# Kernel tuning notes

Measured on AMD Instinct MI355X. Metric: run time of the kernel, lower is better.

The kernel has to match this reference:

```python
import jax, jax.numpy as jnp
import numpy as np

H = 64       # hidden_size
V = 200000   # vocab_size
B = 1024     # batch (sessions)
N = 50       # unique nodes per session graph
S = 50       # session sequence length


def setup_inputs() -> dict:
    key = jax.random.key(0)
    ks = jax.random.split(key, 24)
    s = 0.05
    lin = lambda k, i, o: jax.random.normal(k, (i, o), jnp.float32) * s  # stored [in,out]
    return {
        "alias_inputs": jax.random.randint(ks[0], (B, S), 0, N),
        "ain": jax.random.uniform(ks[1], (B, N, N), jnp.float32) * 0.1,
        "aou": jax.random.uniform(ks[2], (B, N, N), jnp.float32) * 0.1,
        "items": jax.random.randint(ks[3], (B, N), 0, V),
        "mask": jnp.ones((B, S), jnp.int32),
        "edge_index": jnp.zeros((2, 1), jnp.int32),
        "emb": jax.random.normal(ks[4], (V, H), jnp.float32) * s,
        "ein_w": lin(ks[5], H, H), "ein_b": jnp.zeros((H,), jnp.float32),
        "eou_w": lin(ks[6], H, H), "eou_b": jnp.zeros((H,), jnp.float32),
        "b_iah": jax.random.normal(ks[7], (H,), jnp.float32) * s,
        "b_oah": jax.random.normal(ks[8], (H,), jnp.float32) * s,
        "igate_w": lin(ks[9], 2 * H, 3 * H), "igate_b": jnp.zeros((3 * H,), jnp.float32),
        "hgate_w": lin(ks[10], H, 3 * H), "hgate_b": jnp.zeros((3 * H,), jnp.float32),
        "fc1_w": lin(ks[11], H, H), "fc1_b": jnp.zeros((H,), jnp.float32),
        "fc2_w": lin(ks[12], H, H), "fc2_b": jnp.zeros((H,), jnp.float32),
        "fc3_w": lin(ks[13], H, 1),
    }


def _forward(alias_inputs, ain, aou, items, mask, emb,
             ein_w, ein_b, eou_w, eou_b, b_iah, b_oah,
             igate_w, igate_b, hgate_w, hgate_b,
             fc1_w, fc1_b, fc2_w, fc2_b, fc3_w):
    STEP = 1
    h = emb[items]  # [B,N,H]
    for _ in range(STEP):
        # GRU-style gated graph conv cell
        input_in = jnp.matmul(ain, h @ ein_w + ein_b) + b_iah    # [B,N,H]
        input_out = jnp.matmul(aou, h @ eou_w + eou_b) + b_oah   # [B,N,H]
        inputs = jnp.concatenate([input_in, input_out], axis=-1)  # [B,N,2H]
        gi = inputs @ igate_w + igate_b                          # [B,N,3H]
        gh = h @ hgate_w + hgate_b                               # [B,N,3H]
        i_r, i_i, i_n = jnp.split(gi, 3, axis=-1)
        h_r, h_i, h_n = jnp.split(gh, 3, axis=-1)
        resetgate = jax.nn.sigmoid(i_r + h_r)
        inputgate = jax.nn.sigmoid(i_i + h_i)
        newgate = jnp.tanh(i_n + resetgate * h_n)
        h = newgate + inputgate * (h - newgate)
    # batch_emb: gather node states back to sequence order
    seq = jnp.take_along_axis(h, alias_inputs[..., None], axis=1)  # [B,S,H]
    # attention readout
    last = jnp.sum(mask, axis=1) - 1                               # [B]
    ht = seq[jnp.arange(seq.shape[0]), last]                       # [B,H]
    q1 = (ht @ fc1_w + fc1_b)[:, None, :]                          # [B,1,H]
    q2 = seq @ fc2_w + fc2_b                                       # [B,S,H]
    alpha = jax.nn.sigmoid(q1 + q2) @ fc3_w                        # [B,S,1]
    a = jnp.sum(alpha * seq * mask[..., None].astype(seq.dtype), axis=1)  # [B,H]
    return a @ emb[1:].T                                           # [B,V-1]


def reference(alias_inputs, ain, aou, items, mask, edge_index, emb,
              ein_w, ein_b, eou_w, eou_b, b_iah, b_oah,
              igate_w, igate_b, hgate_w, hgate_b,
              fc1_w, fc1_b, fc2_w, fc2_b, fc3_w):
    del edge_index  # unused in the original forward
    return _forward(alias_inputs, ain, aou, items, mask, emb,
                    ein_w, ein_b, eou_w, eou_b, b_iah, b_oah,
                    igate_w, igate_b, hgate_w, hgate_b,
                    fc1_w, fc1_b, fc2_w, fc2_b, fc3_w)
```

## Files before the change

kernel.cpp:

```cpp
#include <hip/hip_runtime.h>
#include <math.h>

#define H 64
#define N 50
#define S 50
#define B 1024
#define V 200000
#define VO (V - 1)

__global__ __launch_bounds__(256) void k1_embed_lin(
    const int* __restrict__ items, const float* __restrict__ emb,
    const float* __restrict__ ein_w, const float* __restrict__ ein_b,
    const float* __restrict__ eou_w, const float* __restrict__ eou_b,
    float* __restrict__ h0, float* __restrict__ hv_in, float* __restrict__ hv_out)
{
    int tid = threadIdx.x;
    int j = tid & 63, w = tid >> 6;
    int bn0 = blockIdx.x * 32;
    __shared__ __align__(16) float hs[32][H];

    for (int idx = tid; idx < 32 * H; idx += 256) {
        int row = idx >> 6, col = idx & 63;
        int item = items[bn0 + row];
        float hv = emb[(size_t)item * H + col];
        hs[row][col] = hv;
        h0[(size_t)(bn0 + row) * H + col] = hv;
    }
    __syncthreads();

    float accI[8], accO[8];
    {
        float bi = ein_b[j], bo = eou_b[j];
        #pragma unroll
        for (int r = 0; r < 8; r++) { accI[r] = bi; accO[r] = bo; }
    }
    int base = w * 8;
    #pragma unroll 4
    for (int k4 = 0; k4 < 16; k4++) {
        float4 xv[8];
        #pragma unroll
        for (int r = 0; r < 8; r++)
            xv[r] = *(const float4*)&hs[base + r][k4 * 4];
        #pragma unroll
        for (int kk = 0; kk < 4; kk++) {
            int k = k4 * 4 + kk;
            float wi = ein_w[k * H + j];
            float wo = eou_w[k * H + j];
            #pragma unroll
            for (int r = 0; r < 8; r++) {
                float x = ((const float*)&xv[r])[kk];
                accI[r] += x * wi;
                accO[r] += x * wo;
            }
        }
    }
    #pragma unroll
    for (int r = 0; r < 8; r++) {
        hv_in [(size_t)(bn0 + base + r) * H + j] = accI[r];
        hv_out[(size_t)(bn0 + base + r) * H + j] = accO[r];
    }
}

__global__ __launch_bounds__(256) void k2_adj(
    const float* __restrict__ ain, const float* __restrict__ aou,
    const float* __restrict__ hv_in, const float* __restrict__ hv_out,
    const float* __restrict__ b_iah, const float* __restrict__ b_oah,
    float* __restrict__ in_in, float* __restrict__ in_out)
{
    int tid = threadIdx.x;
    int j = tid & 63, w = tid >> 6;
    int b = blockIdx.x;
    __shared__ float hin_s[N][H];
    __shared__ float hou_s[N][H];

    for (int idx = tid; idx < N * H; idx += 256) {
        int row = idx >> 6, col = idx & 63;
        hin_s[row][col] = hv_in [((size_t)b * N + row) * H + col];
        hou_s[row][col] = hv_out[((size_t)b * N + row) * H + col];
    }
    __syncthreads();

    float bi = b_iah[j], bo = b_oah[j];
    for (int n = w; n < N; n += 4) {
        const float* ar = ain + ((size_t)b * N + n) * N;
        const float* br = aou + ((size_t)b * N + n) * N;
        float si = bi, so = bo;
        for (int m = 0; m < N; m++) {
            si += ar[m] * hin_s[m][j];
            so += br[m] * hou_s[m][j];
        }
        in_in [((size_t)b * N + n) * H + j] = si;
        in_out[((size_t)b * N + n) * H + j] = so;
    }
}

__global__ __launch_bounds__(256) void k3_gru(
    const float* __restrict__ in_in, const float* __restrict__ in_out,
    const float* __restrict__ igate_w, const float* __restrict__ igate_b,
    const float* __restrict__ hgate_w, const float* __restrict__ hgate_b,
    float* __restrict__ h0)
{
    int tid = threadIdx.x;
    int j = tid & 63, w = tid >> 6;
    int bn0 = blockIdx.x * 32;
    __shared__ __align__(16) float inp_s[32][2 * H];
    __shared__ __align__(16) float h_s[32][H];

    for (int idx = tid; idx < 32 * H; idx += 256) {
        int row = idx >> 6, col = idx & 63;
        size_t g = (size_t)(bn0 + row) * H + col;
        inp_s[row][col]     = in_in[g];
        inp_s[row][H + col] = in_out[g];
        h_s[row][col]       = h0[g];
    }
    __syncthreads();

    int base = w * 8;
    float gr[8], gi[8], gn[8];
    {
        float b0v = igate_b[j], b1v = igate_b[H + j], b2v = igate_b[2 * H + j];
        #pragma unroll
        for (int r = 0; r < 8; r++) { gr[r] = b0v; gi[r] = b1v; gn[r] = b2v; }
    }
    #pragma unroll 2
    for (int k4 = 0; k4 < 32; k4++) {
        float4 xv[8];
        #pragma unroll
        for (int r = 0; r < 8; r++)
            xv[r] = *(const float4*)&inp_s[base + r][k4 * 4];
        #pragma unroll
        for (int kk = 0; kk < 4; kk++) {
            int k = k4 * 4 + kk;
            const float* wrow = igate_w + (size_t)k * 3 * H;
            float w0 = wrow[j], w1 = wrow[H + j], w2 = wrow[2 * H + j];
            #pragma unroll
            for (int r = 0; r < 8; r++) {
                float x = ((const float*)&xv[r])[kk];
                gr[r] += x * w0; gi[r] += x * w1; gn[r] += x * w2;
            }
        }
    }
    float hr[8], hi[8], hn[8];
    {
        float b0v = hgate_b[j], b1v = hgate_b[H + j], b2v = hgate_b[2 * H + j];
        #pragma unroll
        for (int r = 0; r < 8; r++) { hr[r] = b0v; hi[r] = b1v; hn[r] = b2v; }
    }
    #pragma unroll 2
    for (int k4 = 0; k4 < 16; k4++) {
        float4 xv[8];
        #pragma unroll
        for (int r = 0; r < 8; r++)
            xv[r] = *(const float4*)&h_s[base + r][k4 * 4];
        #pragma unroll
        for (int kk = 0; kk < 4; kk++) {
            int k = k4 * 4 + kk;
            const float* wrow = hgate_w + (size_t)k * 3 * H;
            float w0 = wrow[j], w1 = wrow[H + j], w2 = wrow[2 * H + j];
            #pragma unroll
            for (int r = 0; r < 8; r++) {
                float x = ((const float*)&xv[r])[kk];
                hr[r] += x * w0; hi[r] += x * w1; hn[r] += x * w2;
            }
        }
    }
    #pragma unroll
    for (int r = 0; r < 8; r++) {
        float resetg = 1.f / (1.f + expf(-(gr[r] + hr[r])));
        float inputg = 1.f / (1.f + expf(-(gi[r] + hi[r])));
        float newg = tanhf(gn[r] + resetg * hn[r]);
        float h = h_s[base + r][j];
        h0[(size_t)(bn0 + base + r) * H + j] = newg + inputg * (h - newg);
    }
}

__global__ __launch_bounds__(256) void k4_attn(
    const int* __restrict__ alias_in, const int* __restrict__ mask,
    const float* __restrict__ h,
    const float* __restrict__ fc1_w, const float* __restrict__ fc1_b,
    const float* __restrict__ fc2_w, const float* __restrict__ fc2_b,
    const float* __restrict__ fc3_w, float* __restrict__ a)
{
    int tid = threadIdx.x;
    int j = tid & 63, w = tid >> 6;
    int b = blockIdx.x;
    __shared__ __align__(16) float seq_s[S][H];
    __shared__ float f2s[H][H];
    __shared__ float q1s[H];
    __shared__ float apart[4][H];
    __shared__ int msum_s;

    for (int idx = tid; idx < S * H; idx += 256) {
        int s = idx >> 6, c = idx & 63;
        int node = alias_in[b * S + s];
        seq_s[s][c] = h[((size_t)b * N + node) * H + c];
    }
    for (int idx = tid; idx < H * H; idx += 256)
        f2s[idx >> 6][idx & 63] = fc2_w[idx];
    if (tid == 0) {
        int m = 0;
        for (int s = 0; s < S; s++) m += mask[b * S + s];
        msum_s = m;
    }
    __syncthreads();

    int last = msum_s - 1;
    if (w == 0) {
        float q1 = fc1_b[j];
        for (int k = 0; k < H; k++) q1 += seq_s[last][k] * fc1_w[k * H + j];
        q1s[j] = q1;
    }
    __syncthreads();

    float f3 = fc3_w[j];
    float q1v = q1s[j];
    float aj = 0.f;
    for (int s = w; s < S; s += 4) {
        float q2 = fc2_b[j];
        #pragma unroll 4
        for (int k4 = 0; k4 < 16; k4++) {
            float4 sv = *(const float4*)&seq_s[s][k4 * 4];
            q2 += sv.x * f2s[k4 * 4 + 0][j] + sv.y * f2s[k4 * 4 + 1][j]
                + sv.z * f2s[k4 * 4 + 2][j] + sv.w * f2s[k4 * 4 + 3][j];
        }
        float v = (1.f / (1.f + expf(-(q1v + q2)))) * f3;
        #pragma unroll
        for (int off = 1; off < 64; off <<= 1) v += __shfl_xor(v, off, 64);
        aj += v * seq_s[s][j] * (float)mask[b * S + s];
    }
    apart[w][j] = aj;
    __syncthreads();
    if (w == 0)
        a[b * H + j] = apart[0][j] + apart[1][j] + apart[2][j] + apart[3][j];
}

__global__ __launch_bounds__(256) void k5_out(
    const float* __restrict__ a, const float* __restrict__ emb,
    float* __restrict__ out)
{
    __shared__ __align__(16) float As[128][68];
    __shared__ __align__(16) float Es[128][68];
    int tid = threadIdx.x;
    int tx = tid & 15, ty = tid >> 4;
    int v0 = blockIdx.x * 128;
    int b0 = blockIdx.y * 128;

    for (int idx = tid; idx < 128 * 16; idx += 256) {
        int row = idx >> 4, k4 = idx & 15;
        *(float4*)&As[row][k4 * 4] =
            *(const float4*)(a + (size_t)(b0 + row) * H + k4 * 4);
        int v = v0 + row;
        float4 ev = make_float4(0.f, 0.f, 0.f, 0.f);
        if (v < VO) ev = *(const float4*)(emb + (size_t)(v + 1) * H + k4 * 4);
        *(float4*)&Es[row][k4 * 4] = ev;
    }
    __syncthreads();

    float acc[8][8] = {};
    #pragma unroll 2
    for (int k4 = 0; k4 < 16; k4++) {
        float4 af[8], ef[8];
        #pragma unroll
        for (int i = 0; i < 8; i++)
            af[i] = *(const float4*)&As[ty + 16 * i][k4 * 4];
        #pragma unroll
        for (int jj = 0; jj < 8; jj++)
            ef[jj] = *(const float4*)&Es[tx + 16 * jj][k4 * 4];
        #pragma unroll
        for (int i = 0; i < 8; i++)
            #pragma unroll
            for (int jj = 0; jj < 8; jj++)
                acc[i][jj] += af[i].x * ef[jj].x + af[i].y * ef[jj].y +
                              af[i].z * ef[jj].z + af[i].w * ef[jj].w;
    }

    if (v0 + 128 <= VO) {
        #pragma unroll
        for (int i = 0; i < 8; i++) {
            size_t bofs = (size_t)(b0 + ty + 16 * i) * VO;
            #pragma unroll
            for (int jj = 0; jj < 8; jj++)
                out[bofs + v0 + tx + 16 * jj] = acc[i][jj];
        }
    } else {
        #pragma unroll
        for (int i = 0; i < 8; i++) {
            size_t bofs = (size_t)(b0 + ty + 16 * i) * VO;
            #pragma unroll
            for (int jj = 0; jj < 8; jj++) {
                int v = v0 + tx + 16 * jj;
                if (v < VO) out[bofs + v] = acc[i][jj];
            }
        }
    }
}

extern "C" void kernel_launch(void* const* d_in, const int* in_sizes, int n_in,
                              void* d_out, int out_size, void* d_ws, size_t ws_size,
                              hipStream_t stream)
{
    const int*   alias_in = (const int*)d_in[0];
    const float* ain      = (const float*)d_in[1];
    const float* aou      = (const float*)d_in[2];
    const int*   items    = (const int*)d_in[3];
    const int*   mask     = (const int*)d_in[4];
    const float* emb      = (const float*)d_in[6];
    const float* ein_w    = (const float*)d_in[7];
    const float* ein_b    = (const float*)d_in[8];
    const float* eou_w    = (const float*)d_in[9];
    const float* eou_b    = (const float*)d_in[10];
    const float* b_iah    = (const float*)d_in[11];
    const float* b_oah    = (const float*)d_in[12];
    const float* igate_w  = (const float*)d_in[13];
    const float* igate_b  = (const float*)d_in[14];
    const float* hgate_w  = (const float*)d_in[15];
    const float* hgate_b  = (const float*)d_in[16];
    const float* fc1_w    = (const float*)d_in[17];
    const float* fc1_b    = (const float*)d_in[18];
    const float* fc2_w    = (const float*)d_in[19];
    const float* fc2_b    = (const float*)d_in[20];
    const float* fc3_w    = (const float*)d_in[21];

    float* out = (float*)d_out;

    const size_t NH = (size_t)B * N * H;
    float* h0     = out;
    float* hv_in  = h0 + NH;
    float* hv_out = hv_in + NH;
    float* in_in  = hv_out + NH;
    float* in_out = in_in + NH;
    float* a      = (float*)d_ws;

    k1_embed_lin<<<(B * N) / 32, 256, 0, stream>>>(items, emb, ein_w, ein_b,
                                                   eou_w, eou_b, h0, hv_in, hv_out);
    k2_adj<<<B, 256, 0, stream>>>(ain, aou, hv_in, hv_out, b_iah, b_oah,
                                  in_in, in_out);
    k3_gru<<<(B * N) / 32, 256, 0, stream>>>(in_in, in_out, igate_w, igate_b,
                                             hgate_w, hgate_b, h0);
    k4_attn<<<B, 256, 0, stream>>>(alias_in, mask, h0, fc1_w, fc1_b,
                                   fc2_w, fc2_b, fc3_w, a);
    dim3 g5((VO + 127) / 128, B / 128);
    k5_out<<<g5, 256, 0, stream>>>(a, emb, out);
}
```

Measured before the change: 1.413 ms.

## Use split-bf16 MFMA for the final vocab projection GEMM

The output projection a @ emb[1:].T now runs on MFMA matrix cores instead of FP32 FMAs. Each fp32 operand is split into a bf16 high part and a bf16 low residual, and three cross products (hi*hi, lo*hi, hi*lo) are accumulated with the 16x16x32 bf16 MFMA to approximate fp32 accuracy. The goal is to cut the compute cost of the large B x V GEMM. In exchange the staging loop does extra conversion work, and the result is slightly less accurate than a full fp32 product. The output is about 800 MB of fp32 writes, so store bandwidth may still set the runtime.

Measured after the change: 1.314 ms. 1.08x faster.

```diff
diff --git a/kernel.cpp b/kernel.cpp
--- a/kernel.cpp
+++ b/kernel.cpp
@@ -7,6 +7,20 @@
 #define B 1024
 #define V 200000
 #define VO (V - 1)
+
+typedef __attribute__((ext_vector_type(8))) short short8v;
+typedef __attribute__((ext_vector_type(4))) short short4v;
+typedef __attribute__((ext_vector_type(4))) float f32x4;
+
+__device__ __forceinline__ unsigned short f2bf(float x) {
+    union { float f; unsigned int u; } c; c.f = x;
+    unsigned int u = c.u + (0x7fffu + ((c.u >> 16) & 1u));
+    return (unsigned short)(u >> 16);
+}
+__device__ __forceinline__ float bf2f(unsigned short h) {
+    union { float f; unsigned int u; } c; c.u = ((unsigned int)h) << 16;
+    return c.f;
+}
 
 __global__ __launch_bounds__(256) void k1_embed_lin(
     const int* __restrict__ items, const float* __restrict__ emb,
@@ -238,58 +252,100 @@
     const float* __restrict__ a, const float* __restrict__ emb,
     float* __restrict__ out)
 {
-    __shared__ __align__(16) float As[128][68];
-    __shared__ __align__(16) float Es[128][68];
+    __shared__ short As[128][136];
+    __shared__ short Es[128][136];
     int tid = threadIdx.x;
-    int tx = tid & 15, ty = tid >> 4;
     int v0 = blockIdx.x * 128;
     int b0 = blockIdx.y * 128;
 
     for (int idx = tid; idx < 128 * 16; idx += 256) {
         int row = idx >> 4, k4 = idx & 15;
-        *(float4*)&As[row][k4 * 4] =
-            *(const float4*)(a + (size_t)(b0 + row) * H + k4 * 4);
+        float4 av = *(const float4*)(a + (size_t)(b0 + row) * H + k4 * 4);
+        {
+            unsigned short h0b = f2bf(av.x), h1b = f2bf(av.y),
+                           h2b = f2bf(av.z), h3b = f2bf(av.w);
+            short4v hi = { (short)h0b, (short)h1b, (short)h2b, (short)h3b };
+            short4v lo = { (short)f2bf(av.x - bf2f(h0b)),
+                           (short)f2bf(av.y - bf2f(h1b)),
+                           (short)f2bf(av.z - bf2f(h2b)),
+                           (short)f2bf(av.w - bf2f(h3b)) };
+            *(short4v*)&As[row][k4 * 4]      = hi;
+            *(short4v*)&As[row][64 + k4 * 4] = lo;
+        }
         int v = v0 + row;
         float4 ev = make_float4(0.f, 0.f, 0.f, 0.f);
         if (v < VO) ev = *(const float4*)(emb + (size_t)(v + 1) * H + k4 * 4);
-        *(float4*)&Es[row][k4 * 4] = ev;
-    }
-    __syncthreads();
-
-    float acc[8][8] = {};
-    #pragma unroll 2
-    for (int k4 = 0; k4 < 16; k4++) {
-        float4 af[8], ef[8];
-        #pragma unroll
-        for (int i = 0; i < 8; i++)
-            af[i] = *(const float4*)&As[ty + 16 * i][k4 * 4];
-        #pragma unroll
-        for (int jj = 0; jj < 8; jj++)
-            ef[jj] = *(const float4*)&Es[tx + 16 * jj][k4 * 4];
-        #pragma unroll
-        for (int i = 0; i < 8; i++)
+        {
+            unsigned short h0b = f2bf(ev.x), h1b = f2bf(ev.y),
+                           h2b = f2bf(ev.z), h3b = f2bf(ev.w);
+            short4v hi = { (short)h0b, (short)h1b, (short)h2b, (short)h3b };
+            short4v lo = { (short)f2bf(ev.x - bf2f(h0b)),
+                           (short)f2bf(ev.y - bf2f(h1b)),
+                           (short)f2bf(ev.z - bf2f(h2b)),
+                           (short)f2bf(ev.w - bf2f(h3b)) };
+            *(short4v*)&Es[row][k4 * 4]      = hi;
+            *(short4v*)&Es[row][64 + k4 * 4] = lo;
+        }
+    }
+    __syncthreads();
+
+    int lane = tid & 63, wid = tid >> 6;
+    int wv = wid & 1, wb = wid >> 1;
+    int lr = lane & 15, lk = lane >> 4;
+    const short* Ab = &As[wb * 64 + lr][lk * 8];
+    const short* Eb = &Es[wv * 64 + lr][lk * 8];
+
+    f32x4 acc[4][4] = {};
+
+#define KSTEP(AH, AK, EH, EK)                                                  \
+    do {                                                                       \
+        short8v af[4], ef[4];                                                  \
+        _Pragma("unroll")                                                      \
+        for (int i = 0; i < 4; i++)                                            \
+            af[i] = *(const short8v*)(Ab + i * 16 * 136 + (AH) * 64 + (AK) * 32); \
+        _Pragma("unroll")                                                      \
+        for (int jj = 0; jj < 4; jj++)                                         \
+            ef[jj] = *(const short8v*)(Eb + jj * 16 * 136 + (EH) * 64 + (EK) * 32); \
+        _Pragma("unroll")                                                      \
+        for (int i = 0; i < 4; i++)                                            \
+            _Pragma("unroll")                                                  \
+            for (int jj = 0; jj < 4; jj++)                                     \
+                acc[i][jj] = __builtin_amdgcn_mfma_f32_16x16x32_bf16(          \
+                    af[i], ef[jj], acc[i][jj], 0, 0, 0);                       \
+    } while (0)
+
+    KSTEP(0, 0, 0, 0);
+    KSTEP(0, 1, 0, 1);
+    KSTEP(1, 0, 0, 0);
+    KSTEP(1, 1, 0, 1);
+    KSTEP(0, 0, 1, 0);
+    KSTEP(0, 1, 1, 1);
+#undef KSTEP
+
+    if (v0 + 128 <= VO) {
+        #pragma unroll
+        for (int i = 0; i < 4; i++) {
+            int brow = b0 + wb * 64 + i * 16 + lk * 4;
             #pragma unroll
-            for (int jj = 0; jj < 8; jj++)
-                acc[i][jj] += af[i].x * ef[jj].x + af[i].y * ef[jj].y +
-                              af[i].z * ef[jj].z + af[i].w * ef[jj].w;
-    }
-
-    if (v0 + 128 <= VO) {
-        #pragma unroll
-        for (int i = 0; i < 8; i++) {
-            size_t bofs = (size_t)(b0 + ty + 16 * i) * VO;
+            for (int r = 0; r < 4; r++) {
+                size_t ofs = (size_t)(brow + r) * VO + v0 + wv * 64 + lr;
+                #pragma unroll
+                for (int jj = 0; jj < 4; jj++)
+                    out[ofs + jj * 16] = acc[i][jj][r];
+            }
+        }
+    } else {
+        #pragma unroll
+        for (int i = 0; i < 4; i++) {
+            int brow = b0 + wb * 64 + i * 16 + lk * 4;
             #pragma unroll
-            for (int jj = 0; jj < 8; jj++)
-                out[bofs + v0 + tx + 16 * jj] = acc[i][jj];
-        }
-    } else {
-        #pragma unroll
-        for (int i = 0; i < 8; i++) {
-            size_t bofs = (size_t)(b0 + ty + 16 * i) * VO;
-            #pragma unroll
-            for (int jj = 0; jj < 8; jj++) {
-                int v = v0 + tx + 16 * jj;
-                if (v < VO) out[bofs + v] = acc[i][jj];
+            for (int r = 0; r < 4; r++) {
+                size_t ofs = (size_t)(brow + r) * VO;
+                #pragma unroll
+                for (int jj = 0; jj < 4; jj++) {
+                    int v = v0 + wv * 64 + jj * 16 + lr;
+                    if (v < VO) out[ofs + v] = acc[i][jj][r];
+                }
             }
         }
     }
```
